# Kernel tuning notes

Measured on AMD Instinct MI355X. Metric: run time of the kernel, lower is better.

## Reference

```python
import jax, jax.numpy as jnp
import numpy as np

WSCALE = 0.05  # keep qk logits in a stable range for softmax

def setup_inputs() -> dict:
    key = jax.random.key(0)
    ks = jax.random.split(key, 7)
    B, C, H, W = 8, 256, 64, 64
    d = C // 8
    x = jax.random.normal(ks[0], (B, C, H, W), dtype=jnp.float32)
    Wq = jax.random.normal(ks[1], (d, C), dtype=jnp.float32) * WSCALE
    Wk = jax.random.normal(ks[2], (d, C), dtype=jnp.float32) * WSCALE
    Wv = jax.random.normal(ks[3], (C, C), dtype=jnp.float32) * WSCALE
    bq = jnp.zeros((d,), jnp.float32)
    bk = jnp.zeros((d,), jnp.float32)
    bv = jnp.zeros((C,), jnp.float32)
    return {"x": x, "Wq": Wq, "bq": bq, "Wk": Wk, "bk": bk, "Wv": Wv, "bv": bv}

def reference(x, Wq, bq, Wk, bk, Wv, bv):
    B, C, H, W = x.shape
    N = H * W
    xf = x.reshape(B, C, N)                                  # [B,C,N]
    # 1x1 convs == per-pixel linear projections
    q = jnp.einsum('dc,bcn->bdn', Wq, xf) + bq[None, :, None]  # [B,d,N]
    k = jnp.einsum('dc,bcn->bdn', Wk, xf) + bk[None, :, None]  # [B,d,N]
    v = jnp.einsum('ec,bcn->ben', Wv, xf) + bv[None, :, None]  # [B,C,N]
    # attn[b,i,j] = q_i . k_j ; softmax over j (keys)
    attn = jax.nn.softmax(jnp.einsum('bdi,bdj->bij', q, k), axis=-1)  # [B,N,N]
    # out[b,c,i] = sum_j v[b,c,j] * attn[b,i,j]
    out = jnp.einsum('bcj,bij->bci', v, attn)                # [B,C,N]
    return out.reshape(B, C, H, W)
```

## Files before the change

### kernel.cpp

```cpp
#include <hip/hip_runtime.h>
#include <math.h>

#define NB 8
#define NC 256
#define ND 32
#define NN 4096
#define NM 320
#define LOG2E 1.44269504088896f
#define PSTRIDE 264

typedef short short8 __attribute__((ext_vector_type(8)));
typedef float f32x4 __attribute__((ext_vector_type(4)));

__device__ __forceinline__ unsigned int f2bf_u(float f) {
    return (__float_as_uint(f) + 0x8000u) >> 16;
}
__device__ __forceinline__ unsigned short f2bf(float f) {
    return (unsigned short)f2bf_u(f);
}

__global__ __launch_bounds__(256) void repack_kernel(
    const float* __restrict__ Wq, const float* __restrict__ bq,
    const float* __restrict__ Wk, const float* __restrict__ bk,
    const float* __restrict__ Wv, const float* __restrict__ bv,
    unsigned short* __restrict__ wp, float* __restrict__ bias)
{
    const int T    = blockIdx.x * 256 + threadIdx.x;
    const int j    = T & 7;
    const int lane = (T >> 3) & 63;
    const int ks   = (T >> 9) & 7;
    const int mt   = T >> 12;
    const int m = mt * 16 + (lane & 15);
    const int k = ks * 32 + ((lane >> 4) << 3) + j;
    float wv;
    if (m < 32)       wv = Wq[m * NC + k] * LOG2E;
    else if (m < 64)  wv = Wk[(m - 32) * NC + k];
    else              wv = Wv[(m - 64) * NC + k];
    wp[T] = f2bf(wv);
    if (T < NM) {
        float bb;
        if (T < 32)      bb = bq[T] * LOG2E;
        else if (T < 64) bb = bk[T - 32];
        else             bb = bv[T - 64];
        bias[T] = bb;
    }
}

__global__ __launch_bounds__(256, 2) void proj_kernel(
    const float* __restrict__ x,
    const unsigned short* __restrict__ wp,
    const float* __restrict__ bias,
    unsigned short* __restrict__ q_ws,
    unsigned short* __restrict__ k_ws,
    unsigned short* __restrict__ v_ws)
{
    __shared__ __align__(16) unsigned short xs[64 * PSTRIDE];

    const int b  = blockIdx.x >> 6;
    const int n0 = (blockIdx.x & 63) << 6;
    const int w    = threadIdx.x >> 6;
    const int lane = threadIdx.x & 63;
    const int li = lane & 15;
    const int qd = lane >> 4;

    {
        const float* xb = x + ((size_t)b * NC) * NN + n0;
        const int n = threadIdx.x & 63;
        #pragma unroll 8
        for (int it = 0; it < 64; ++it) {
            const int c = w + 4 * it;
            xs[n * PSTRIDE + c] = f2bf(xb[(size_t)c * NN + n]);
        }
    }
    __syncthreads();

    f32x4 acc[5][4];
    #pragma unroll
    for (int u = 0; u < 5; ++u) {
        const int mt = w + 4 * u;
        const f32x4 b4 = *(const f32x4*)(bias + mt * 16 + qd * 4);
        #pragma unroll
        for (int nf = 0; nf < 4; ++nf) acc[u][nf] = b4;
    }

    #pragma unroll
    for (int ks = 0; ks < 8; ++ks) {
        short8 bf[4];
        #pragma unroll
        for (int nf = 0; nf < 4; ++nf)
            bf[nf] = *(const short8*)(xs + (nf * 16 + li) * PSTRIDE + ks * 32 + qd * 8);
        #pragma unroll
        for (int u = 0; u < 5; ++u) {
            const int mt = w + 4 * u;
            const short8 af = *(const short8*)(wp + (size_t)((mt * 8 + ks) * 64 + lane) * 8);
            #pragma unroll
            for (int nf = 0; nf < 4; ++nf)
                acc[u][nf] = __builtin_amdgcn_mfma_f32_16x16x32_bf16(af, bf[nf], acc[u][nf], 0, 0, 0);
        }
    }

    #pragma unroll
    for (int u = 0; u < 5; ++u) {
        const int mt = w + 4 * u;
        if (mt < 4) {
            unsigned short* dst = (mt < 2) ? q_ws : k_ws;
            const int d0 = (mt & 1) * 16 + qd * 4;
            #pragma unroll
            for (int nf = 0; nf < 4; ++nf) {
                const int n = n0 + nf * 16 + li;
                uint2 pk;
                pk.x = (f2bf_u(acc[u][nf][1]) << 16) | f2bf_u(acc[u][nf][0]);
                pk.y = (f2bf_u(acc[u][nf][3]) << 16) | f2bf_u(acc[u][nf][2]);
                *(uint2*)(dst + ((size_t)b * NN + n) * ND + d0) = pk;
            }
        } else {
            const int c0 = (mt - 4) * 16 + qd * 4;
            #pragma unroll
            for (int nf = 0; nf < 4; ++nf) {
                const int n = n0 + nf * 16 + li;
                #pragma unroll
                for (int r = 0; r < 4; ++r)
                    v_ws[((size_t)b * NC + c0 + r) * NN + n] = f2bf(acc[u][nf][r]);
            }
        }
    }
}

__global__ __launch_bounds__(256, 2) void attn_kernel(
    const unsigned short* __restrict__ q_ws,
    const unsigned short* __restrict__ k_ws,
    const unsigned short* __restrict__ v_ws,
    float* __restrict__ out)
{
    __shared__ __align__(16) unsigned short Pbuf[4][4][16*72];

    const int b  = blockIdx.x & 7;
    const int i0 = (blockIdx.x >> 3) * 64;
    const int w    = threadIdx.x >> 6;
    const int lane = threadIdx.x & 63;
    const int li = lane & 15;
    const int qd = lane >> 4;
    const int q8 = qd * 8;
    const int q4 = qd * 4;

    const unsigned short* kb = k_ws + (size_t)b * NN * ND + (size_t)li * ND + q8;

    short8 qf[4];
    #pragma unroll
    for (int sb = 0; sb < 4; ++sb)
        qf[sb] = *(const short8*)(q_ws + ((size_t)b*NN + i0 + 16*sb + li)*ND + q8);

    const unsigned short* vb[4];
    #pragma unroll
    for (int nt = 0; nt < 4; ++nt)
        vb[nt] = v_ws + ((size_t)b*NC + w*64 + nt*16 + li)*NN + q8;

    f32x4 o[4][4];
    #pragma unroll
    for (int sb = 0; sb < 4; ++sb)
        #pragma unroll
        for (int nt = 0; nt < 4; ++nt)
            o[sb][nt] = (f32x4){0.f,0.f,0.f,0.f};
    float l[4] = {0.f,0.f,0.f,0.f};
    const f32x4 z4 = {0.f,0.f,0.f,0.f};

    for (int j0 = 0; j0 < NN; j0 += 64) {
        short8 kf[4];
        #pragma unroll
        for (int t = 0; t < 4; ++t)
            kf[t] = *(const short8*)(kb + (size_t)(j0 + 16*t) * ND);
        short8 vf[4][2];
        #pragma unroll
        for (int nt = 0; nt < 4; ++nt)
            #pragma unroll
            for (int ks = 0; ks < 2; ++ks)
                vf[nt][ks] = *(const short8*)(vb[nt] + j0 + 32*ks);

        #pragma unroll
        for (int sb = 0; sb < 4; ++sb) {
            f32x4 s[4];
            #pragma unroll
            for (int t = 0; t < 4; ++t)
                s[t] = __builtin_amdgcn_mfma_f32_16x16x32_bf16(kf[t], qf[sb], z4, 0, 0, 0);
            float lsum = 0.f;
            unsigned short* Pw = &Pbuf[w][sb][li*72 + q4];
            #pragma unroll
            for (int t = 0; t < 4; ++t) {
                const float p0 = __builtin_amdgcn_exp2f(s[t][0]);
                const float p1 = __builtin_amdgcn_exp2f(s[t][1]);
                const float p2 = __builtin_amdgcn_exp2f(s[t][2]);
                const float p3 = __builtin_amdgcn_exp2f(s[t][3]);
                lsum += (p0 + p1) + (p2 + p3);
                const unsigned u0 = __float_as_uint(p0) + 0x8000u;
                const unsigned u1 = __float_as_uint(p1) + 0x8000u;
                const unsigned u2 = __float_as_uint(p2) + 0x8000u;
                const unsigned u3 = __float_as_uint(p3) + 0x8000u;
                uint2 pk;
                pk.x = __builtin_amdgcn_perm(u1, u0, 0x07060302u);
                pk.y = __builtin_amdgcn_perm(u3, u2, 0x07060302u);
                *(uint2*)(Pw + 16*t) = pk;
            }
            lsum += __shfl_xor(lsum, 16, 64);
            lsum += __shfl_xor(lsum, 32, 64);
            l[sb] += lsum;
        }

        asm volatile("s_waitcnt lgkmcnt(0)" ::: "memory");

        #pragma unroll
        for (int sb = 0; sb < 4; ++sb) {
            const unsigned short* Pr = &Pbuf[w][sb][li*72 + q8];
            const short8 pf0 = *(const short8*)(Pr);
            const short8 pf1 = *(const short8*)(Pr + 32);
            #pragma unroll
            for (int nt = 0; nt < 4; ++nt) {
                o[sb][nt] = __builtin_amdgcn_mfma_f32_16x16x32_bf16(vf[nt][0], pf0, o[sb][nt], 0, 0, 0);
                o[sb][nt] = __builtin_amdgcn_mfma_f32_16x16x32_bf16(vf[nt][1], pf1, o[sb][nt], 0, 0, 0);
            }
        }
    }

    #pragma unroll
    for (int sb = 0; sb < 4; ++sb) {
        const float linv = 1.0f / l[sb];
        #pragma unroll
        for (int nt = 0; nt < 4; ++nt) {
            const int c = w*64 + nt*16 + q4;
            float* op = out + ((size_t)b*NC + c)*NN + i0 + 16*sb + li;
            #pragma unroll
            for (int r = 0; r < 4; ++r)
                op[(size_t)r * NN] = o[sb][nt][r] * linv;
        }
    }
}

extern "C" void kernel_launch(void* const* d_in, const int* in_sizes, int n_in,
                              void* d_out, int out_size, void* d_ws, size_t ws_size,
                              hipStream_t stream) {
    const float* x  = (const float*)d_in[0];
    const float* Wq = (const float*)d_in[1];
    const float* bq = (const float*)d_in[2];
    const float* Wk = (const float*)d_in[3];
    const float* bk = (const float*)d_in[4];
    const float* Wv = (const float*)d_in[5];
    const float* bv = (const float*)d_in[6];
    float* out = (float*)d_out;

    unsigned short* q_ws = (unsigned short*)d_ws;
    unsigned short* k_ws = q_ws + (size_t)NB * NN * ND;
    unsigned short* v_ws = k_ws + (size_t)NB * NN * ND;
    unsigned short* wp   = v_ws + (size_t)NB * NC * NN;
    float*          bias = (float*)(wp + (size_t)NM * NC);

    repack_kernel<<<NM * NC / 256, 256, 0, stream>>>(Wq, bq, Wk, bk, Wv, bv, wp, bias);
    proj_kernel<<<NB * (NN / 64), 256, 0, stream>>>(x, wp, bias, q_ws, k_ws, v_ws);
    attn_kernel<<<NB * (NN / 64), 256, 0, stream>>>(q_ws, k_ws, v_ws, out);
}
```

Baseline: 257.6 us.

## Share QK scores across waves via double-buffered LDS and shrink projection tile

The attention kernel moves to 512 threads. The eight waves split the score computation so that each query-subblock/key-half pair is computed once. The bf16 probabilities go into a double-buffered, rotation-swizzled shared tile, and every wave then multiplies them against its own 32-channel slice of V. This removes the four-fold redundant QK MFMA and exp2 work of the old layout, at the cost of a block-wide barrier every key tile and a cross-wave row-sum reduction at the end. The projection kernel also halves its pixel tile to 32, packs four channels per LDS store when converting x, and requests higher occupancy.

Measured after the change: 248.8 us. 1.04x faster.

```diff
diff --git a/kernel.cpp b/kernel.cpp
--- a/kernel.cpp
+++ b/kernel.cpp
@@ -7,7 +7,7 @@
 #define NN 4096
 #define NM 320
 #define LOG2E 1.44269504088896f
-#define PSTRIDE 264
+#define XSTR 264
 
 typedef short short8 __attribute__((ext_vector_type(8)));
 typedef float f32x4 __attribute__((ext_vector_type(4)));
@@ -46,7 +46,7 @@
     }
 }
 
-__global__ __launch_bounds__(256, 2) void proj_kernel(
+__global__ __launch_bounds__(256, 4) void proj_kernel(
     const float* __restrict__ x,
     const unsigned short* __restrict__ wp,
     const float* __restrict__ bias,
@@ -54,48 +54,56 @@
     unsigned short* __restrict__ k_ws,
     unsigned short* __restrict__ v_ws)
 {
-    __shared__ __align__(16) unsigned short xs[64 * PSTRIDE];
-
-    const int b  = blockIdx.x >> 6;
-    const int n0 = (blockIdx.x & 63) << 6;
-    const int w    = threadIdx.x >> 6;
-    const int lane = threadIdx.x & 63;
+    __shared__ __align__(16) unsigned short xs[32 * XSTR];
+
+    const int b  = blockIdx.x >> 7;
+    const int n0 = (blockIdx.x & 127) << 5;
+    const int t  = threadIdx.x;
+
+    {
+        const int n  = t & 31;
+        const int cg = t >> 5;
+        const float* xb = x + (size_t)b * NC * NN + n0 + n;
+        #pragma unroll
+        for (int it = 0; it < 8; ++it) {
+            const int c = 32 * it + 4 * cg;
+            const float x0 = xb[(size_t)(c + 0) * NN];
+            const float x1 = xb[(size_t)(c + 1) * NN];
+            const float x2 = xb[(size_t)(c + 2) * NN];
+            const float x3 = xb[(size_t)(c + 3) * NN];
+            uint2 pk;
+            pk.x = (f2bf_u(x1) << 16) | f2bf_u(x0);
+            pk.y = (f2bf_u(x3) << 16) | f2bf_u(x2);
+            *(uint2*)(xs + n * XSTR + c) = pk;
+        }
+    }
+    __syncthreads();
+
+    const int w    = t >> 6;
+    const int lane = t & 63;
     const int li = lane & 15;
     const int qd = lane >> 4;
 
-    {
-        const float* xb = x + ((size_t)b * NC) * NN + n0;
-        const int n = threadIdx.x & 63;
-        #pragma unroll 8
-        for (int it = 0; it < 64; ++it) {
-            const int c = w + 4 * it;
-            xs[n * PSTRIDE + c] = f2bf(xb[(size_t)c * NN + n]);
-        }
-    }
-    __syncthreads();
-
-    f32x4 acc[5][4];
+    f32x4 acc[5][2];
     #pragma unroll
     for (int u = 0; u < 5; ++u) {
         const int mt = w + 4 * u;
         const f32x4 b4 = *(const f32x4*)(bias + mt * 16 + qd * 4);
-        #pragma unroll
-        for (int nf = 0; nf < 4; ++nf) acc[u][nf] = b4;
+        acc[u][0] = b4; acc[u][1] = b4;
     }
 
     #pragma unroll
     for (int ks = 0; ks < 8; ++ks) {
-        short8 bf[4];
-        #pragma unroll
-        for (int nf = 0; nf < 4; ++nf)
-            bf[nf] = *(const short8*)(xs + (nf * 16 + li) * PSTRIDE + ks * 32 + qd * 8);
+        short8 bf[2];
+        #pragma unroll
+        for (int nf = 0; nf < 2; ++nf)
+            bf[nf] = *(const short8*)(xs + (nf * 16 + li) * XSTR + ks * 32 + qd * 8);
         #pragma unroll
         for (int u = 0; u < 5; ++u) {
             const int mt = w + 4 * u;
             const short8 af = *(const short8*)(wp + (size_t)((mt * 8 + ks) * 64 + lane) * 8);
-            #pragma unroll
-            for (int nf = 0; nf < 4; ++nf)
-                acc[u][nf] = __builtin_amdgcn_mfma_f32_16x16x32_bf16(af, bf[nf], acc[u][nf], 0, 0, 0);
+            acc[u][0] = __builtin_amdgcn_mfma_f32_16x16x32_bf16(af, bf[0], acc[u][0], 0, 0, 0);
+            acc[u][1] = __builtin_amdgcn_mfma_f32_16x16x32_bf16(af, bf[1], acc[u][1], 0, 0, 0);
         }
     }
 
@@ -106,7 +114,7 @@
             unsigned short* dst = (mt < 2) ? q_ws : k_ws;
             const int d0 = (mt & 1) * 16 + qd * 4;
             #pragma unroll
-            for (int nf = 0; nf < 4; ++nf) {
+            for (int nf = 0; nf < 2; ++nf) {
                 const int n = n0 + nf * 16 + li;
                 uint2 pk;
                 pk.x = (f2bf_u(acc[u][nf][1]) << 16) | f2bf_u(acc[u][nf][0]);
@@ -116,7 +124,7 @@
         } else {
             const int c0 = (mt - 4) * 16 + qd * 4;
             #pragma unroll
-            for (int nf = 0; nf < 4; ++nf) {
+            for (int nf = 0; nf < 2; ++nf) {
                 const int n = n0 + nf * 16 + li;
                 #pragma unroll
                 for (int r = 0; r < 4; ++r)
@@ -126,112 +134,108 @@
     }
 }
 
-__global__ __launch_bounds__(256, 2) void attn_kernel(
+__global__ __launch_bounds__(512, 4) void attn_kernel(
     const unsigned short* __restrict__ q_ws,
     const unsigned short* __restrict__ k_ws,
     const unsigned short* __restrict__ v_ws,
     float* __restrict__ out)
 {
-    __shared__ __align__(16) unsigned short Pbuf[4][4][16*72];
+    __shared__ __align__(16) unsigned short Pb[2][4][16 * 64];
+    __shared__ float lred[8][16];
 
     const int b  = blockIdx.x & 7;
     const int i0 = (blockIdx.x >> 3) * 64;
-    const int w    = threadIdx.x >> 6;
-    const int lane = threadIdx.x & 63;
+    const int t  = threadIdx.x;
+    const int w    = t >> 6;
+    const int lane = t & 63;
     const int li = lane & 15;
     const int qd = lane >> 4;
-    const int q8 = qd * 8;
-    const int q4 = qd * 4;
-
-    const unsigned short* kb = k_ws + (size_t)b * NN * ND + (size_t)li * ND + q8;
-
-    short8 qf[4];
+    const int sw = w & 3;
+    const int th = w >> 2;
+    const int c0 = w * 32;
+    const int rot = (li & 3) << 2;
+
+    const int wblk0 = ((8 * th + 0 + qd) + rot) & 15;
+    const int wblk1 = ((8 * th + 4 + qd) + rot) & 15;
+    const int rblk0 = ((2 * qd) + rot) & 15;
+    const int rblk1 = ((8 + 2 * qd) + rot) & 15;
+
+    const short8 qf = *(const short8*)(q_ws + ((size_t)b * NN + i0 + 16 * sw + li) * ND + qd * 8);
+    const unsigned short* kb = k_ws + (size_t)b * NN * ND + (size_t)li * ND + qd * 8
+                             + (size_t)(16 * 2 * th) * ND;
+    const unsigned short* vb0 = v_ws + ((size_t)b * NC + c0 + li) * NN + qd * 8;
+    const unsigned short* vb1 = vb0 + (size_t)16 * NN;
+
+    f32x4 o[4][2];
+    #pragma unroll
+    for (int sb = 0; sb < 4; ++sb) { o[sb][0] = (f32x4){0,0,0,0}; o[sb][1] = (f32x4){0,0,0,0}; }
+    float l_loc = 0.f;
+    const f32x4 z4 = {0.f, 0.f, 0.f, 0.f};
+
+    int buf = 0;
+    for (int j0 = 0; j0 < NN; j0 += 64) {
+        const short8 kf0 = *(const short8*)(kb + (size_t)j0 * ND);
+        const short8 kf1 = *(const short8*)(kb + (size_t)(j0 + 16) * ND);
+        short8 vf[2][2];
+        #pragma unroll
+        for (int ks = 0; ks < 2; ++ks) {
+            vf[0][ks] = *(const short8*)(vb0 + j0 + 32 * ks);
+            vf[1][ks] = *(const short8*)(vb1 + j0 + 32 * ks);
+        }
+
+        unsigned short* Pw = &Pb[buf][sw][li * 64];
+        #pragma unroll
+        for (int tt = 0; tt < 2; ++tt) {
+            const f32x4 s = __builtin_amdgcn_mfma_f32_16x16x32_bf16(tt ? kf1 : kf0, qf, z4, 0, 0, 0);
+            const float p0 = __builtin_amdgcn_exp2f(s[0]);
+            const float p1 = __builtin_amdgcn_exp2f(s[1]);
+            const float p2 = __builtin_amdgcn_exp2f(s[2]);
+            const float p3 = __builtin_amdgcn_exp2f(s[3]);
+            l_loc += (p0 + p1) + (p2 + p3);
+            const unsigned u0 = __float_as_uint(p0) + 0x8000u;
+            const unsigned u1 = __float_as_uint(p1) + 0x8000u;
+            const unsigned u2 = __float_as_uint(p2) + 0x8000u;
+            const unsigned u3 = __float_as_uint(p3) + 0x8000u;
+            uint2 pk;
+            pk.x = __builtin_amdgcn_perm(u1, u0, 0x07060302u);
+            pk.y = __builtin_amdgcn_perm(u3, u2, 0x07060302u);
+            *(uint2*)(Pw + (tt ? wblk1 : wblk0) * 4) = pk;
+        }
+
+        __syncthreads();
+
+        #pragma unroll
+        for (int sb = 0; sb < 4; ++sb) {
+            const unsigned short* Pr = &Pb[buf][sb][li * 64];
+            const short8 pf0 = *(const short8*)(Pr + rblk0 * 4);
+            const short8 pf1 = *(const short8*)(Pr + rblk1 * 4);
+            o[sb][0] = __builtin_amdgcn_mfma_f32_16x16x32_bf16(vf[0][0], pf0, o[sb][0], 0, 0, 0);
+            o[sb][0] = __builtin_amdgcn_mfma_f32_16x16x32_bf16(vf[0][1], pf1, o[sb][0], 0, 0, 0);
+            o[sb][1] = __builtin_amdgcn_mfma_f32_16x16x32_bf16(vf[1][0], pf0, o[sb][1], 0, 0, 0);
+            o[sb][1] = __builtin_amdgcn_mfma_f32_16x16x32_bf16(vf[1][1], pf1, o[sb][1], 0, 0, 0);
+        }
+        buf ^= 1;
+    }
+
+    l_loc += __shfl_xor(l_loc, 16, 64);
+    l_loc += __shfl_xor(l_loc, 32, 64);
+    if (lane < 16) lred[w][lane] = l_loc;
+    __syncthreads();
+    float linv[4];
     #pragma unroll
     for (int sb = 0; sb < 4; ++sb)
-        qf[sb] = *(const short8*)(q_ws + ((size_t)b*NN + i0 + 16*sb + li)*ND + q8);
-
-    const unsigned short* vb[4];
-    #pragma unroll
-    for (int nt = 0; nt < 4; ++nt)
-        vb[nt] = v_ws + ((size_t)b*NC + w*64 + nt*16 + li)*NN + q8;
-
-    f32x4 o[4][4];
+        linv[sb] = 1.0f / (lred[sb][li] + lred[sb + 4][li]);
+
     #pragma unroll
     for (int sb = 0; sb < 4; ++sb)
         #pragma unroll
-        for (int nt = 0; nt < 4; ++nt)
-            o[sb][nt] = (f32x4){0.f,0.f,0.f,0.f};
-    float l[4] = {0.f,0.f,0.f,0.f};
-    const f32x4 z4 = {0.f,0.f,0.f,0.f};
-
-    for (int j0 = 0; j0 < NN; j0 += 64) {
-        short8 kf[4];
-        #pragma unroll
-        for (int t = 0; t < 4; ++t)
-            kf[t] = *(const short8*)(kb + (size_t)(j0 + 16*t) * ND);
-        short8 vf[4][2];
-        #pragma unroll
-        for (int nt = 0; nt < 4; ++nt)
-            #pragma unroll
-            for (int ks = 0; ks < 2; ++ks)
-                vf[nt][ks] = *(const short8*)(vb[nt] + j0 + 32*ks);
-
-        #pragma unroll
-        for (int sb = 0; sb < 4; ++sb) {
-            f32x4 s[4];
-            #pragma unroll
-            for (int t = 0; t < 4; ++t)
-                s[t] = __builtin_amdgcn_mfma_f32_16x16x32_bf16(kf[t], qf[sb], z4, 0, 0, 0);
-            float lsum = 0.f;
-            unsigned short* Pw = &Pbuf[w][sb][li*72 + q4];
-            #pragma unroll
-            for (int t = 0; t < 4; ++t) {
-                const float p0 = __builtin_amdgcn_exp2f(s[t][0]);
-                const float p1 = __builtin_amdgcn_exp2f(s[t][1]);
-                const float p2 = __builtin_amdgcn_exp2f(s[t][2]);
-                const float p3 = __builtin_amdgcn_exp2f(s[t][3]);
-                lsum += (p0 + p1) + (p2 + p3);
-                const unsigned u0 = __float_as_uint(p0) + 0x8000u;
-                const unsigned u1 = __float_as_uint(p1) + 0x8000u;
-                const unsigned u2 = __float_as_uint(p2) + 0x8000u;
-                const unsigned u3 = __float_as_uint(p3) + 0x8000u;
-                uint2 pk;
-                pk.x = __builtin_amdgcn_perm(u1, u0, 0x07060302u);
-                pk.y = __builtin_amdgcn_perm(u3, u2, 0x07060302u);
-                *(uint2*)(Pw + 16*t) = pk;
-            }
-            lsum += __shfl_xor(lsum, 16, 64);
-            lsum += __shfl_xor(lsum, 32, 64);
-            l[sb] += lsum;
-        }
-
-        asm volatile("s_waitcnt lgkmcnt(0)" ::: "memory");
-
-        #pragma unroll
-        for (int sb = 0; sb < 4; ++sb) {
-            const unsigned short* Pr = &Pbuf[w][sb][li*72 + q8];
-            const short8 pf0 = *(const short8*)(Pr);
-            const short8 pf1 = *(const short8*)(Pr + 32);
-            #pragma unroll
-            for (int nt = 0; nt < 4; ++nt) {
-                o[sb][nt] = __builtin_amdgcn_mfma_f32_16x16x32_bf16(vf[nt][0], pf0, o[sb][nt], 0, 0, 0);
-                o[sb][nt] = __builtin_amdgcn_mfma_f32_16x16x32_bf16(vf[nt][1], pf1, o[sb][nt], 0, 0, 0);
-            }
-        }
-    }
-
-    #pragma unroll
-    for (int sb = 0; sb < 4; ++sb) {
-        const float linv = 1.0f / l[sb];
-        #pragma unroll
-        for (int nt = 0; nt < 4; ++nt) {
-            const int c = w*64 + nt*16 + q4;
-            float* op = out + ((size_t)b*NC + c)*NN + i0 + 16*sb + li;
+        for (int nt = 0; nt < 2; ++nt) {
+            const int c = c0 + nt * 16 + qd * 4;
+            float* op = out + ((size_t)b * NC + c) * NN + i0 + 16 * sb + li;
             #pragma unroll
             for (int r = 0; r < 4; ++r)
-                op[(size_t)r * NN] = o[sb][nt][r] * linv;
-        }
-    }
+                op[(size_t)r * NN] = o[sb][nt][r] * linv[sb];
+        }
 }
 
 extern "C" void kernel_launch(void* const* d_in, const int* in_sizes, int n_in,
@@ -253,6 +257,6 @@
     float*          bias = (float*)(wp + (size_t)NM * NC);
 
     repack_kernel<<<NM * NC / 256, 256, 0, stream>>>(Wq, bq, Wk, bk, Wv, bv, wp, bias);
-    proj_kernel<<<NB * (NN / 64), 256, 0, stream>>>(x, wp, bias, q_ws, k_ws, v_ws);
-    attn_kernel<<<NB * (NN / 64), 256, 0, stream>>>(q_ws, k_ws, v_ws, out);
-}
+    proj_kernel<<<NB * (NN / 32), 256, 0, stream>>>(x, wp, bias, q_ws, k_ws, v_ws);
+    attn_kernel<<<NB * (NN / 64), 512, 0, stream>>>(q_ws, k_ws, v_ws, out);
+}
```
